# Performance work log

Measured on AMD Instinct MI355X. Metric: run time of the kernel, lower is better.

The kernel has to match this reference:

```python
import jax, jax.numpy as jnp
import numpy as np

B, T_TXT, T_IMG, N_LAT = 4, 2048, 8, 64
DIM, DIM_VIS, HEADS, DIM_HEAD = 2048, 1024, 8, 64
INNER = HEADS * DIM_HEAD
LN_EPS = 1e-5


def setup_inputs() -> dict:
    key = jax.random.key(0)
    ks = jax.random.split(key, 8)
    x = jax.random.normal(ks[0], (B, T_TXT, DIM), dtype=jnp.float32)
    media = jax.random.normal(ks[1], (B, T_IMG, N_LAT, DIM_VIS), dtype=jnp.float32)
    # exactly T_IMG media tokens per batch row at random positions
    pos = jax.random.randint(ks[2], (B, T_IMG), 0, T_TXT)
    media_locations = jnp.zeros((B, T_TXT), dtype=bool).at[jnp.arange(B)[:, None], pos].set(True)
    gamma = jnp.ones((DIM,), dtype=jnp.float32)
    beta = jnp.zeros((DIM,), dtype=jnp.float32)
    Wq = jax.random.normal(ks[3], (DIM, INNER), dtype=jnp.float32) * 0.02
    Wkv = jax.random.normal(ks[4], (DIM_VIS, 2 * INNER), dtype=jnp.float32) * 0.02
    Wout = jax.random.normal(ks[5], (INNER, DIM), dtype=jnp.float32) * 0.02
    return {"x": x, "media": media, "media_locations": media_locations,
            "gamma": gamma, "beta": beta, "Wq": Wq, "Wkv": Wkv, "Wout": Wout}


def _split_heads(t, h):
    b, s, _ = t.shape
    return t.reshape(b, s, h, -1).transpose(0, 2, 1, 3)  # b h s d


def reference(x, media, media_locations, gamma, beta, Wq, Wkv, Wout):
    b, t_txt, _ = x.shape
    _, t_img, n, _ = media.shape
    scale = DIM_HEAD ** (-0.5)

    # LayerNorm
    mu = jnp.mean(x, axis=-1, keepdims=True)
    var = jnp.mean(jnp.square(x - mu), axis=-1, keepdims=True)
    xn = (x - mu) * jax.lax.rsqrt(var + LN_EPS) * gamma + beta

    q = _split_heads(xn @ Wq, HEADS) * scale                # b h i d
    media_f = media.reshape(b, t_img * n, -1)               # b (t n) dv
    kv = media_f @ Wkv
    k, v = jnp.split(kv, 2, axis=-1)
    k = _split_heads(k, HEADS)                              # b h j d
    v = _split_heads(v, HEADS)

    sim = jnp.einsum('bhid,bhjd->bhij', q, k)               # b h i (t n)

    text_time = jnp.cumsum(media_locations.astype(jnp.int32), axis=-1)   # b i
    media_time = jnp.repeat(jnp.arange(1, t_img + 1), n)                 # (t n)
    mask = text_time[:, None, :, None] == media_time[None, None, None, :]

    neg = -jnp.finfo(sim.dtype).max
    sim = jnp.where(mask, sim, neg)
    sim = sim - jax.lax.stop_gradient(jnp.max(sim, axis=-1, keepdims=True))
    attn = jax.nn.softmax(sim, axis=-1)
    # zero attention for text tokens that precede any media
    attn = jnp.where((text_time == 0)[:, None, :, None], 0.0, attn)

    out = jnp.einsum('bhij,bhjd->bhid', attn, v)
    out = out.transpose(0, 2, 1, 3).reshape(b, t_txt, INNER)
    return out @ Wout
```

## Files before the change

kernel.cpp:

```cpp
#include <hip/hip_runtime.h>
#include <hip/hip_bf16.h>
#include <stdint.h>

typedef __bf16 bf16_t;
typedef __bf16 bf16x8 __attribute__((ext_vector_type(8)));
typedef float f32x4 __attribute__((ext_vector_type(4)));

#define NB      4
#define T_TXT   2048
#define T_IMG   8
#define N_LAT   64
#define DIM     2048
#define DIM_VIS 1024
#define HEADS   8
#define DHEAD   64
#define INNER   512

__device__ __forceinline__ void gld_lds16(const void* g, void* l) {
    __builtin_amdgcn_global_load_lds((const __attribute__((address_space(1))) void*)g,
                                     (__attribute__((address_space(3))) void*)l,
                                     16, 0, 0);
}

__global__ __launch_bounds__(256) void transpose3_k(const float* __restrict__ Wq,
                                                    const float* __restrict__ Wkv,
                                                    const float* __restrict__ Wout,
                                                    bf16_t* __restrict__ WqT,
                                                    bf16_t* __restrict__ WkvT,
                                                    bf16_t* __restrict__ WoutT) {
    __shared__ float tile[32][33];
    const float* in; bf16_t* out; int R, C;
    int which = blockIdx.y;
    if (which == 0)      { in = Wq;   out = WqT;   R = 2048; C = 512;  }
    else if (which == 1) { in = Wkv;  out = WkvT;  R = 1024; C = 1024; }
    else                 { in = Wout; out = WoutT; R = 512;  C = 2048; }
    int nbx = C >> 5;
    int bx = blockIdx.x % nbx, by = blockIdx.x / nbx;
    int c0 = bx * 32, r0 = by * 32;
    int x = threadIdx.x, y = threadIdx.y;
#pragma unroll
    for (int d = 0; d < 4; d++)
        tile[y + d * 8][x] = in[(size_t)(r0 + y + d * 8) * C + c0 + x];
    __syncthreads();
#pragma unroll
    for (int d = 0; d < 4; d++)
        out[(size_t)(c0 + y + d * 8) * R + r0 + x] = (bf16_t)tile[x][y + d * 8];
}

__global__ __launch_bounds__(256) void cvt_k(const float* __restrict__ in,
                                             bf16_t* __restrict__ out) {
    int idx = (blockIdx.x * 256 + threadIdx.x) * 8;
    f32x4 a = *(const f32x4*)(in + idx);
    f32x4 b = *(const f32x4*)(in + idx + 4);
    bf16x8 o;
#pragma unroll
    for (int i = 0; i < 4; i++) { o[i] = (bf16_t)a[i]; o[i + 4] = (bf16_t)b[i]; }
    *(bf16x8*)(out + idx) = o;
}

__global__ __launch_bounds__(256) void ln_k(const float* __restrict__ x,
                                            const float* __restrict__ gamma,
                                            const float* __restrict__ beta,
                                            bf16_t* __restrict__ xn) {
    int row = blockIdx.x;
    int t = threadIdx.x;
    const float* xp = x + (size_t)row * DIM + t * 8;
    f32x4 v0 = *(const f32x4*)xp;
    f32x4 v1 = *(const f32x4*)(xp + 4);
    float f[8];
    float s = 0.f, ss = 0.f;
#pragma unroll
    for (int i = 0; i < 4; i++) { f[i] = v0[i]; f[i + 4] = v1[i]; }
#pragma unroll
    for (int i = 0; i < 8; i++) { s += f[i]; ss += f[i] * f[i]; }
#pragma unroll
    for (int off = 32; off > 0; off >>= 1) { s += __shfl_xor(s, off); ss += __shfl_xor(ss, off); }
    __shared__ float sbuf[4], sbuf2[4];
    int wid = t >> 6, lane = t & 63;
    if (lane == 0) { sbuf[wid] = s; sbuf2[wid] = ss; }
    __syncthreads();
    s  = sbuf[0] + sbuf[1] + sbuf[2] + sbuf[3];
    ss = sbuf2[0] + sbuf2[1] + sbuf2[2] + sbuf2[3];
    float mu  = s * (1.0f / DIM);
    float var = ss * (1.0f / DIM) - mu * mu;
    float rs  = rsqrtf(var + 1e-5f);
    f32x4 g0 = *(const f32x4*)(gamma + t * 8);
    f32x4 g1 = *(const f32x4*)(gamma + t * 8 + 4);
    f32x4 b0 = *(const f32x4*)(beta + t * 8);
    f32x4 b1 = *(const f32x4*)(beta + t * 8 + 4);
    bf16x8 o;
#pragma unroll
    for (int i = 0; i < 4; i++) {
        o[i]     = (bf16_t)((f[i]     - mu) * rs * g0[i] + b0[i]);
        o[i + 4] = (bf16_t)((f[i + 4] - mu) * rs * g1[i] + b1[i]);
    }
    *(bf16x8*)(xn + (size_t)row * DIM + t * 8) = o;
}

template <typename OT>
__device__ __forceinline__ void gemm_body256(const bf16_t* __restrict__ A,
                                             const bf16_t* __restrict__ Bt,
                                             OT* __restrict__ C,
                                             int M, int N, int K, int Kper,
                                             float scale, int bid,
                                             int gx, int gy, int gz,
                                             bf16_t* lA, bf16_t* lB) {
    int tid = threadIdx.x;
    int w = tid >> 6, lane = tid & 63;
    int wm = w >> 2, wn = w & 3;

    int nwg = gx * gy * gz;
    int cpx = nwg >> 3;
    int nid = (bid & 7) * cpx + (bid >> 3);
    int tpy = gx * gz;
    int by = nid / tpy;
    int rr = nid - by * tpy;
    int bz = rr / gx;
    int bx = rr - bz * gx;

    int bm0 = by * 256, bn0 = bx * 256;
    int kbase = bz * Kper;
    int q = lane >> 4, l16 = lane & 15;

    const bf16_t* pA0 = A  + (size_t)(bm0 + w * 32      + l16) * K + kbase + q * 8;
    const bf16_t* pA1 = A  + (size_t)(bm0 + w * 32 + 16 + l16) * K + kbase + q * 8;
    const bf16_t* pB0 = Bt + (size_t)(bn0 + w * 32      + l16) * K + kbase + q * 8;
    const bf16_t* pB1 = Bt + (size_t)(bn0 + w * 32 + 16 + l16) * K + kbase + q * 8;

    f32x4 acc[8][4];
#pragma unroll
    for (int i = 0; i < 8; i++)
#pragma unroll
        for (int j = 0; j < 4; j++)
            acc[i][j] = (f32x4){0.f, 0.f, 0.f, 0.f};

    auto stage = [&](int t) {
        int buf = t & 3;
        int k0 = t << 5;
        gld_lds16(pA0 + k0, lA + buf * 8192 + (w * 2)     * 512);
        gld_lds16(pA1 + k0, lA + buf * 8192 + (w * 2 + 1) * 512);
        gld_lds16(pB0 + k0, lB + buf * 8192 + (w * 2)     * 512);
        gld_lds16(pB1 + k0, lB + buf * 8192 + (w * 2 + 1) * 512);
    };
    auto compute = [&](int t, bool dostage) {
        int buf = t & 3;
        bf16x8 af[8], bfr[4];
#pragma unroll
        for (int mt = 0; mt < 8; mt++)
            af[mt] = *(const bf16x8*)(lA + buf * 8192 + (wm * 8 + mt) * 512 + q * 128 + l16 * 8);
#pragma unroll
        for (int nt = 0; nt < 4; nt++)
            bfr[nt] = *(const bf16x8*)(lB + buf * 8192 + (wn * 4 + nt) * 512 + q * 128 + l16 * 8);
        if (dostage) stage(t + 3);
        __builtin_amdgcn_s_setprio(1);
#pragma unroll
        for (int mt = 0; mt < 8; mt++)
#pragma unroll
            for (int nt = 0; nt < 4; nt++)
                acc[mt][nt] = __builtin_amdgcn_mfma_f32_16x16x32_bf16(af[mt], bfr[nt], acc[mt][nt], 0, 0, 0);
        __builtin_amdgcn_s_setprio(0);
    };

    int nsteps = Kper >> 5;
    stage(0); stage(1); stage(2);
    for (int t = 0; t < nsteps - 2; t++) {
        asm volatile("s_waitcnt vmcnt(8)" ::: "memory");
        __builtin_amdgcn_s_barrier();
        __builtin_amdgcn_sched_barrier(0);
        compute(t, t + 3 < nsteps);
    }
    asm volatile("s_waitcnt vmcnt(4)" ::: "memory");
    __builtin_amdgcn_s_barrier();
    __builtin_amdgcn_sched_barrier(0);
    compute(nsteps - 2, false);
    asm volatile("s_waitcnt vmcnt(0)" ::: "memory");
    __builtin_amdgcn_s_barrier();
    __builtin_amdgcn_sched_barrier(0);
    compute(nsteps - 1, false);

    OT* Cz = C + (size_t)bz * M * N;
#pragma unroll
    for (int mt = 0; mt < 8; mt++)
#pragma unroll
        for (int nt = 0; nt < 4; nt++)
#pragma unroll
            for (int r = 0; r < 4; r++) {
                int row = bm0 + wm * 128 + mt * 16 + q * 4 + r;
                int col = bn0 + wn * 64 + nt * 16 + l16;
                Cz[(size_t)row * N + col] = (OT)(acc[mt][nt][r] * scale);
            }
}

__global__ __launch_bounds__(512, 2) void gemm12_k(const bf16_t* __restrict__ xn,
                                                   const bf16_t* __restrict__ WqT,
                                                   bf16_t* __restrict__ part,
                                                   const bf16_t* __restrict__ mediab,
                                                   const bf16_t* __restrict__ WkvT,
                                                   bf16_t* __restrict__ kvpart) {
    __shared__ __align__(16) bf16_t lA[4 * 8192];
    __shared__ __align__(16) bf16_t lB[4 * 8192];
    int bid = blockIdx.x;
    if (bid < 256)
        gemm_body256<bf16_t>(xn, WqT, part, 8192, 512, 2048, 512, 1.0f, bid, 2, 32, 4, lA, lB);
    else
        gemm_body256<bf16_t>(mediab, WkvT, kvpart, 2048, 1024, 1024, 256, 1.0f, bid - 256, 4, 8, 4, lA, lB);
}

__global__ __launch_bounds__(512, 2) void gemm3_k(const bf16_t* __restrict__ aout,
                                                  const bf16_t* __restrict__ WoutT,
                                                  float* __restrict__ out) {
    __shared__ __align__(16) bf16_t lA[4 * 8192];
    __shared__ __align__(16) bf16_t lB[4 * 8192];
    gemm_body256<float>(aout, WoutT, out, 8192, 2048, 512, 512, 1.0f, blockIdx.x, 8, 32, 1, lA, lB);
}

__global__ __launch_bounds__(256) void reduce4_k(const bf16_t* __restrict__ p,
                                                 bf16_t* __restrict__ o,
                                                 size_t n, float scale) {
    size_t i = ((size_t)blockIdx.x * 256 + threadIdx.x) * 8;
    bf16x8 a0 = *(const bf16x8*)(p + i);
    bf16x8 a1 = *(const bf16x8*)(p + n + i);
    bf16x8 a2 = *(const bf16x8*)(p + 2 * n + i);
    bf16x8 a3 = *(const bf16x8*)(p + 3 * n + i);
    bf16x8 r;
#pragma unroll
    for (int u = 0; u < 8; u++)
        r[u] = (bf16_t)(((float)a0[u] + (float)a1[u] + (float)a2[u] + (float)a3[u]) * scale);
    *(bf16x8*)(o + i) = r;
}

__global__ __launch_bounds__(256) void cumsum_bucket_k(const void* __restrict__ locs,
                                                       int* __restrict__ bstart,
                                                       int* __restrict__ bcnt) {
    int b = blockIdx.x, t = threadIdx.x;
    const unsigned* up = (const unsigned*)locs;
    const int* ip = (const int*)locs;
    const unsigned char* bp = (const unsigned char*)locs;
    const float* fp = (const float*)locs;

    int other = 0, nf = 0;
#pragma unroll
    for (int i = 0; i < 8; i++) {
        unsigned wv = up[t * 8 + i];
        nf    += (wv == 0x3F800000u);
        other += (wv != 0u && wv != 1u && wv != 0x3F800000u);
    }
#pragma unroll
    for (int off = 32; off > 0; off >>= 1) { other += __shfl_xor(other, off); nf += __shfl_xor(nf, off); }
    __shared__ int so[4], sf[4];
    int wid = t >> 6, lane = t & 63;
    if (lane == 0) { so[wid] = other; sf[wid] = nf; }
    __syncthreads();
    other = so[0] + so[1] + so[2] + so[3];
    nf    = sf[0] + sf[1] + sf[2] + sf[3];
    int mode = (other > 0) ? 0 : ((nf > 0) ? 2 : 1);

    int v[8];
    int s = 0;
#pragma unroll
    for (int i = 0; i < 8; i++) {
        int idx = b * T_TXT + t * 8 + i;
        int xv;
        if (mode == 1)      xv = ip[idx];
        else if (mode == 0) xv = (int)bp[idx];
        else                xv = (fp[idx] != 0.f) ? 1 : 0;
        v[i] = xv;
        s += xv;
    }
    __shared__ int sc[256];
    __shared__ int sstart[T_IMG];
    if (t < T_IMG) sstart[t] = T_TXT;
    sc[t] = s;
    __syncthreads();
    for (int off = 1; off < 256; off <<= 1) {
        int add = (t >= off) ? sc[t - off] : 0;
        __syncthreads();
        sc[t] += add;
        __syncthreads();
    }
    int run = sc[t] - s;
#pragma unroll
    for (int i = 0; i < 8; i++) {
        run += v[i];
        if (v[i] && run <= T_IMG) sstart[run - 1] = t * 8 + i;
    }
    __syncthreads();
    if (t < T_IMG) {
        int st = sstart[t];
        int nx = (t + 1 < T_IMG) ? sstart[t + 1] : T_TXT;
        bstart[b * T_IMG + t] = st;
        bcnt[b * T_IMG + t]   = nx - st;
    }
}

__global__ __launch_bounds__(256) void attn_mfma_k(const bf16_t* __restrict__ q,
                                                   const bf16_t* __restrict__ kv,
                                                   const int* __restrict__ bstart,
                                                   const int* __restrict__ bcnt,
                                                   bf16_t* __restrict__ aout) {
    __shared__ __align__(16) bf16_t lK[64 * 64];
    __shared__ __align__(16) bf16_t lVt[64 * 64];
    __shared__ __align__(16) bf16_t lP[4][16 * 64];

    int bid = blockIdx.x;
    int bucket = bid >> 6;
    int h = (bid >> 3) & 7;
    int c = bid & 7;
    int n_q = bcnt[bucket];
    int qlo = c << 8;
    if (n_q <= qlo) return;
    int qhi = (n_q < qlo + 256) ? n_q : (qlo + 256);
    int b = bucket >> 3;
    int timg = bucket & 7;
    int row0 = b * T_TXT + bstart[bucket];
    size_t krow0 = (size_t)(b * (T_IMG * N_LAT) + timg * N_LAT);

    int tid = threadIdx.x;
    int wid = tid >> 6, lane = tid & 63;
    int quad = lane >> 4, l16 = lane & 15;

    {
        const bf16_t* s0 = kv + (krow0 + 16 * wid + (lane >> 3)) * (2 * INNER) + h * DHEAD + (lane & 7) * 8;
        const bf16_t* s1 = kv + (krow0 + 16 * wid + 8 + (lane >> 3)) * (2 * INNER) + h * DHEAD + (lane & 7) * 8;
        gld_lds16(s0, lK + wid * 1024);
        gld_lds16(s1, lK + wid * 1024 + 512);
    }
    {
        int key = tid & 63, dblk = tid >> 6;
        const bf16_t* vsrc = kv + (krow0 + key) * (2 * INNER) + INNER + h * DHEAD + dblk * 16;
        bf16x8 v0 = *(const bf16x8*)vsrc;
        bf16x8 v1 = *(const bf16x8*)(vsrc + 8);
#pragma unroll
        for (int u = 0; u < 8; u++) {
            lVt[(dblk * 16 + u) * 64 + key]     = v0[u];
            lVt[(dblk * 16 + 8 + u) * 64 + key] = v1[u];
        }
    }
    __syncthreads();

    for (int c0 = qlo + wid * 16; c0 < qhi; c0 += 64) {
        int qi = row0 + c0 + ((c0 + l16 < n_q) ? l16 : 0);

        const bf16_t* qrow = q + (size_t)qi * INNER + h * DHEAD + quad * 8;
        bf16x8 qf0 = *(const bf16x8*)qrow;
        bf16x8 qf1 = *(const bf16x8*)(qrow + 32);
        f32x4 s[4];
#pragma unroll
        for (int nt = 0; nt < 4; nt++) s[nt] = (f32x4){0.f, 0.f, 0.f, 0.f};
#pragma unroll
        for (int nt = 0; nt < 4; nt++) {
            bf16x8 kf0 = *(const bf16x8*)(lK + (l16 + 16 * nt) * 64 + quad * 8);
            bf16x8 kf1 = *(const bf16x8*)(lK + (l16 + 16 * nt) * 64 + 32 + quad * 8);
            s[nt] = __builtin_amdgcn_mfma_f32_16x16x32_bf16(qf0, kf0, s[nt], 0, 0, 0);
            s[nt] = __builtin_amdgcn_mfma_f32_16x16x32_bf16(qf1, kf1, s[nt], 0, 0, 0);
        }

        float mr[4];
#pragma unroll
        for (int r = 0; r < 4; r++) {
            float m = fmaxf(fmaxf(s[0][r], s[1][r]), fmaxf(s[2][r], s[3][r]));
#pragma unroll
            for (int off = 8; off >= 1; off >>= 1) m = fmaxf(m, __shfl_xor(m, off));
            mr[r] = m;
        }
        float p[4][4];
#pragma unroll
        for (int nt = 0; nt < 4; nt++)
#pragma unroll
            for (int r = 0; r < 4; r++)
                p[nt][r] = __expf(s[nt][r] - mr[r]);
#pragma unroll
        for (int r = 0; r < 4; r++) {
            float tsum = p[0][r] + p[1][r] + p[2][r] + p[3][r];
#pragma unroll
            for (int off = 8; off >= 1; off >>= 1) tsum += __shfl_xor(tsum, off);
            float inv = 1.0f / tsum;
            p[0][r] *= inv; p[1][r] *= inv; p[2][r] *= inv; p[3][r] *= inv;
        }

        bf16_t* pt = lP[wid];
#pragma unroll
        for (int nt = 0; nt < 4; nt++)
#pragma unroll
            for (int r = 0; r < 4; r++)
                pt[(quad * 4 + r) * 64 + 16 * nt + l16] = (bf16_t)p[nt][r];
        asm volatile("s_waitcnt lgkmcnt(0)" ::: "memory");

        bf16x8 pf0 = *(const bf16x8*)(pt + l16 * 64 + quad * 8);
        bf16x8 pf1 = *(const bf16x8*)(pt + l16 * 64 + 32 + quad * 8);
        f32x4 o[4];
#pragma unroll
        for (int ntd = 0; ntd < 4; ntd++) o[ntd] = (f32x4){0.f, 0.f, 0.f, 0.f};
#pragma unroll
        for (int ntd = 0; ntd < 4; ntd++) {
            bf16x8 vf0 = *(const bf16x8*)(lVt + (l16 + 16 * ntd) * 64 + quad * 8);
            bf16x8 vf1 = *(const bf16x8*)(lVt + (l16 + 16 * ntd) * 64 + 32 + quad * 8);
            o[ntd] = __builtin_amdgcn_mfma_f32_16x16x32_bf16(pf0, vf0, o[ntd], 0, 0, 0);
            o[ntd] = __builtin_amdgcn_mfma_f32_16x16x32_bf16(pf1, vf1, o[ntd], 0, 0, 0);
        }

#pragma unroll
        for (int r = 0; r < 4; r++) {
            int qidx = c0 + quad * 4 + r;
            if (qidx < n_q) {
                bf16_t* op = aout + (size_t)(row0 + qidx) * INNER + h * DHEAD + l16;
#pragma unroll
                for (int ntd = 0; ntd < 4; ntd++)
                    op[16 * ntd] = (bf16_t)o[ntd][r];
            }
        }
    }
}

extern "C" void kernel_launch(void* const* d_in, const int* in_sizes, int n_in,
                              void* d_out, int out_size, void* d_ws, size_t ws_size,
                              hipStream_t stream) {
    const float* x     = (const float*)d_in[0];
    const float* media = (const float*)d_in[1];
    const void*  locs  = d_in[2];
    const float* gamma = (const float*)d_in[3];
    const float* beta  = (const float*)d_in[4];
    const float* Wq    = (const float*)d_in[5];
    const float* Wkv   = (const float*)d_in[6];
    const float* Wout  = (const float*)d_in[7];
    float* out = (float*)d_out;

    bf16_t* xn   = (bf16_t*)d_out;
    bf16_t* part = (bf16_t*)d_out + (size_t)16 * 1024 * 1024;

    char* p = (char*)d_ws;
    bf16_t* qbuf   = (bf16_t*)p; p += (size_t)8192 * 512 * 2;
    bf16_t* aout   = (bf16_t*)p; p += (size_t)8192 * 512 * 2;
    bf16_t* kvbuf  = (bf16_t*)p; p += (size_t)2048 * 1024 * 2;
    bf16_t* mediab = (bf16_t*)p; p += (size_t)2048 * 1024 * 2;
    bf16_t* WqT    = (bf16_t*)p; p += (size_t)512 * 2048 * 2;
    bf16_t* WkvT   = (bf16_t*)p; p += (size_t)1024 * 1024 * 2;
    bf16_t* WoutT  = (bf16_t*)p; p += (size_t)2048 * 512 * 2;
    int*    bstart = (int*)p;    p += 32 * sizeof(int);
    int*    bcnt   = (int*)p;    p += 32 * sizeof(int);

    cumsum_bucket_k<<<NB, 256, 0, stream>>>(locs, bstart, bcnt);
    transpose3_k<<<dim3(1024, 3), dim3(32, 8), 0, stream>>>(Wq, Wkv, Wout, WqT, WkvT, WoutT);
    cvt_k<<<(2048 * 1024) / (256 * 8), 256, 0, stream>>>(media, mediab);

    ln_k<<<8192, 256, 0, stream>>>(x, gamma, beta, xn);

    gemm12_k<<<384, 512, 0, stream>>>(xn, WqT, part, mediab, WkvT, qbuf);

    reduce4_k<<<1024, 256, 0, stream>>>(qbuf, kvbuf, (size_t)2048 * 1024, 1.0f);
    reduce4_k<<<2048, 256, 0, stream>>>(part, qbuf, (size_t)8192 * 512, 0.125f);

    hipMemsetAsync(aout, 0, (size_t)8192 * 512 * 2, stream);

    attn_mfma_k<<<32 * HEADS * 8, 256, 0, stream>>>(qbuf, kvbuf, bstart, bcnt, aout);

    gemm3_k<<<256, 512, 0, stream>>>(aout, WoutT, out);
}
```

Before: 263.4 us.

## Restructure GEMM pipeline to double-buffered K=64 steps with split fragment loads

Replaces the four-stage K=32 ring buffer with a two-buffer scheme holding K=64 per stage. Each stage is processed as two K halves with one barrier per half. Within a half, the A fragments are loaded in two groups of four, and the next stage's global-to-LDS copies are interleaved between the MFMA groups. The aim is fewer register-held fragments and finer interleaving of loads with MFMA work, at the cost of a shallower prefetch distance.

Measured after the change: 263.6 us. No clear change (+0.1%).

```diff
diff --git a/kernel.cpp b/kernel.cpp
--- a/kernel.cpp
+++ b/kernel.cpp
@@ -121,11 +121,12 @@
     int bm0 = by * 256, bn0 = bx * 256;
     int kbase = bz * Kper;
     int q = lane >> 4, l16 = lane & 15;
-
-    const bf16_t* pA0 = A  + (size_t)(bm0 + w * 32      + l16) * K + kbase + q * 8;
-    const bf16_t* pA1 = A  + (size_t)(bm0 + w * 32 + 16 + l16) * K + kbase + q * 8;
-    const bf16_t* pB0 = Bt + (size_t)(bn0 + w * 32      + l16) * K + kbase + q * 8;
-    const bf16_t* pB1 = Bt + (size_t)(bn0 + w * 32 + 16 + l16) * K + kbase + q * 8;
+    int rbase = q * 128 + l16 * 8;
+
+    const bf16_t* sA0 = A  + (size_t)(bm0 + (2 * w) * 16     + l16) * K + kbase + q * 8;
+    const bf16_t* sA1 = A  + (size_t)(bm0 + (2 * w + 1) * 16 + l16) * K + kbase + q * 8;
+    const bf16_t* sB0 = Bt + (size_t)(bn0 + (2 * w) * 16     + l16) * K + kbase + q * 8;
+    const bf16_t* sB1 = Bt + (size_t)(bn0 + (2 * w + 1) * 16 + l16) * K + kbase + q * 8;
 
     f32x4 acc[8][4];
 #pragma unroll
@@ -134,49 +135,86 @@
         for (int j = 0; j < 4; j++)
             acc[i][j] = (f32x4){0.f, 0.f, 0.f, 0.f};
 
-    auto stage = [&](int t) {
-        int buf = t & 3;
-        int k0 = t << 5;
-        gld_lds16(pA0 + k0, lA + buf * 8192 + (w * 2)     * 512);
-        gld_lds16(pA1 + k0, lA + buf * 8192 + (w * 2 + 1) * 512);
-        gld_lds16(pB0 + k0, lB + buf * 8192 + (w * 2)     * 512);
-        gld_lds16(pB1 + k0, lB + buf * 8192 + (w * 2 + 1) * 512);
+    auto stA = [&](int buf, int t, int kh) {
+        int off = t * 64 + kh * 32;
+        bf16_t* d = lA + buf * 16384 + (kh * 16 + 2 * w) * 512;
+        gld_lds16(sA0 + off, d);
+        gld_lds16(sA1 + off, d + 512);
     };
-    auto compute = [&](int t, bool dostage) {
-        int buf = t & 3;
-        bf16x8 af[8], bfr[4];
-#pragma unroll
-        for (int mt = 0; mt < 8; mt++)
-            af[mt] = *(const bf16x8*)(lA + buf * 8192 + (wm * 8 + mt) * 512 + q * 128 + l16 * 8);
-#pragma unroll
-        for (int nt = 0; nt < 4; nt++)
-            bfr[nt] = *(const bf16x8*)(lB + buf * 8192 + (wn * 4 + nt) * 512 + q * 128 + l16 * 8);
-        if (dostage) stage(t + 3);
-        __builtin_amdgcn_s_setprio(1);
-#pragma unroll
-        for (int mt = 0; mt < 8; mt++)
-#pragma unroll
-            for (int nt = 0; nt < 4; nt++)
-                acc[mt][nt] = __builtin_amdgcn_mfma_f32_16x16x32_bf16(af[mt], bfr[nt], acc[mt][nt], 0, 0, 0);
-        __builtin_amdgcn_s_setprio(0);
+    auto stB = [&](int buf, int t, int kh) {
+        int off = t * 64 + kh * 32;
+        bf16_t* d = lB + buf * 16384 + (kh * 16 + 2 * w) * 512;
+        gld_lds16(sB0 + off, d);
+        gld_lds16(sB1 + off, d + 512);
     };
 
-    int nsteps = Kper >> 5;
-    stage(0); stage(1); stage(2);
-    for (int t = 0; t < nsteps - 2; t++) {
-        asm volatile("s_waitcnt vmcnt(8)" ::: "memory");
+    int T = Kper >> 6;
+    stA(0, 0, 0); stB(0, 0, 0);
+    stA(0, 0, 1); stB(0, 0, 1);
+
+    for (int t = 0; t < T; ++t) {
+        int buf = t & 1;
+        int nbuf = buf ^ 1;
+        const bf16_t* LA = lA + buf * 16384;
+        const bf16_t* LB = lB + buf * 16384;
+        bool more = (t + 1 < T);
+
+        asm volatile("s_waitcnt vmcnt(4)" ::: "memory");
         __builtin_amdgcn_s_barrier();
         __builtin_amdgcn_sched_barrier(0);
-        compute(t, t + 3 < nsteps);
-    }
-    asm volatile("s_waitcnt vmcnt(4)" ::: "memory");
-    __builtin_amdgcn_s_barrier();
-    __builtin_amdgcn_sched_barrier(0);
-    compute(nsteps - 2, false);
-    asm volatile("s_waitcnt vmcnt(0)" ::: "memory");
-    __builtin_amdgcn_s_barrier();
-    __builtin_amdgcn_sched_barrier(0);
-    compute(nsteps - 1, false);
+
+        bf16x8 af[4], bfr[4];
+#pragma unroll
+        for (int i = 0; i < 4; i++) af[i]  = *(const bf16x8*)(LA + (wm * 8 + i) * 512 + rbase);
+#pragma unroll
+        for (int j = 0; j < 4; j++) bfr[j] = *(const bf16x8*)(LB + (wn * 4 + j) * 512 + rbase);
+        if (more) stA(nbuf, t + 1, 0);
+        __builtin_amdgcn_s_setprio(1);
+#pragma unroll
+        for (int i = 0; i < 4; i++)
+#pragma unroll
+            for (int j = 0; j < 4; j++)
+                acc[i][j] = __builtin_amdgcn_mfma_f32_16x16x32_bf16(af[i], bfr[j], acc[i][j], 0, 0, 0);
+        __builtin_amdgcn_s_setprio(0);
+#pragma unroll
+        for (int i = 0; i < 4; i++) af[i] = *(const bf16x8*)(LA + (wm * 8 + 4 + i) * 512 + rbase);
+        if (more) stB(nbuf, t + 1, 0);
+        __builtin_amdgcn_s_setprio(1);
+#pragma unroll
+        for (int i = 0; i < 4; i++)
+#pragma unroll
+            for (int j = 0; j < 4; j++)
+                acc[4 + i][j] = __builtin_amdgcn_mfma_f32_16x16x32_bf16(af[i], bfr[j], acc[4 + i][j], 0, 0, 0);
+        __builtin_amdgcn_s_setprio(0);
+
+        if (more) { asm volatile("s_waitcnt vmcnt(4)" ::: "memory"); }
+        else      { asm volatile("s_waitcnt vmcnt(0)" ::: "memory"); }
+        __builtin_amdgcn_s_barrier();
+        __builtin_amdgcn_sched_barrier(0);
+
+#pragma unroll
+        for (int i = 0; i < 4; i++) af[i]  = *(const bf16x8*)(LA + (16 + wm * 8 + i) * 512 + rbase);
+#pragma unroll
+        for (int j = 0; j < 4; j++) bfr[j] = *(const bf16x8*)(LB + (16 + wn * 4 + j) * 512 + rbase);
+        if (more) stA(nbuf, t + 1, 1);
+        __builtin_amdgcn_s_setprio(1);
+#pragma unroll
+        for (int i = 0; i < 4; i++)
+#pragma unroll
+            for (int j = 0; j < 4; j++)
+                acc[i][j] = __builtin_amdgcn_mfma_f32_16x16x32_bf16(af[i], bfr[j], acc[i][j], 0, 0, 0);
+        __builtin_amdgcn_s_setprio(0);
+#pragma unroll
+        for (int i = 0; i < 4; i++) af[i] = *(const bf16x8*)(LA + (16 + wm * 8 + 4 + i) * 512 + rbase);
+        if (more) stB(nbuf, t + 1, 1);
+        __builtin_amdgcn_s_setprio(1);
+#pragma unroll
+        for (int i = 0; i < 4; i++)
+#pragma unroll
+            for (int j = 0; j < 4; j++)
+                acc[4 + i][j] = __builtin_amdgcn_mfma_f32_16x16x32_bf16(af[i], bfr[j], acc[4 + i][j], 0, 0, 0);
+        __builtin_amdgcn_s_setprio(0);
+    }
 
     OT* Cz = C + (size_t)bz * M * N;
 #pragma unroll
@@ -197,8 +235,8 @@
                                                    const bf16_t* __restrict__ mediab,
                                                    const bf16_t* __restrict__ WkvT,
                                                    bf16_t* __restrict__ kvpart) {
-    __shared__ __align__(16) bf16_t lA[4 * 8192];
-    __shared__ __align__(16) bf16_t lB[4 * 8192];
+    __shared__ __align__(16) bf16_t lA[2 * 16384];
+    __shared__ __align__(16) bf16_t lB[2 * 16384];
     int bid = blockIdx.x;
     if (bid < 256)
         gemm_body256<bf16_t>(xn, WqT, part, 8192, 512, 2048, 512, 1.0f, bid, 2, 32, 4, lA, lB);
@@ -209,8 +247,8 @@
 __global__ __launch_bounds__(512, 2) void gemm3_k(const bf16_t* __restrict__ aout,
                                                   const bf16_t* __restrict__ WoutT,
                                                   float* __restrict__ out) {
-    __shared__ __align__(16) bf16_t lA[4 * 8192];
-    __shared__ __align__(16) bf16_t lB[4 * 8192];
+    __shared__ __align__(16) bf16_t lA[2 * 16384];
+    __shared__ __align__(16) bf16_t lB[2 * 16384];
     gemm_body256<float>(aout, WoutT, out, 8192, 2048, 512, 512, 1.0f, blockIdx.x, 8, 32, 1, lA, lB);
 }
 
```

## Merge prep kernels, drop KV split-K reduction, fold memset into reduce

Applied to the files above, without the earlier changes.

Combines the weight transposes, media conversion and location cumsum into one prep kernel. The KV projection now runs without split-K (32 blocks writing kvbuf directly), and those blocks are placed first in the fused GEMM launch, which removes one reduction kernel. Zeroing of the attention output buffer moves into the Q reduction kernel, replacing the memset. The aim is fewer launches and less partial-sum traffic, at the cost of longer per-block K loops for the KV GEMM.

After: 257.8 us. -2.1%, faster.

```diff
diff --git a/kernel.cpp b/kernel.cpp
--- a/kernel.cpp
+++ b/kernel.cpp
@@ -22,40 +22,111 @@
                                      16, 0, 0);
 }
 
-__global__ __launch_bounds__(256) void transpose3_k(const float* __restrict__ Wq,
-                                                    const float* __restrict__ Wkv,
-                                                    const float* __restrict__ Wout,
-                                                    bf16_t* __restrict__ WqT,
-                                                    bf16_t* __restrict__ WkvT,
-                                                    bf16_t* __restrict__ WoutT) {
-    __shared__ float tile[32][33];
-    const float* in; bf16_t* out; int R, C;
-    int which = blockIdx.y;
-    if (which == 0)      { in = Wq;   out = WqT;   R = 2048; C = 512;  }
-    else if (which == 1) { in = Wkv;  out = WkvT;  R = 1024; C = 1024; }
-    else                 { in = Wout; out = WoutT; R = 512;  C = 2048; }
-    int nbx = C >> 5;
-    int bx = blockIdx.x % nbx, by = blockIdx.x / nbx;
-    int c0 = bx * 32, r0 = by * 32;
-    int x = threadIdx.x, y = threadIdx.y;
-#pragma unroll
-    for (int d = 0; d < 4; d++)
-        tile[y + d * 8][x] = in[(size_t)(r0 + y + d * 8) * C + c0 + x];
-    __syncthreads();
-#pragma unroll
-    for (int d = 0; d < 4; d++)
-        out[(size_t)(c0 + y + d * 8) * R + r0 + x] = (bf16_t)tile[x][y + d * 8];
-}
-
-__global__ __launch_bounds__(256) void cvt_k(const float* __restrict__ in,
-                                             bf16_t* __restrict__ out) {
-    int idx = (blockIdx.x * 256 + threadIdx.x) * 8;
-    f32x4 a = *(const f32x4*)(in + idx);
-    f32x4 b = *(const f32x4*)(in + idx + 4);
-    bf16x8 o;
-#pragma unroll
-    for (int i = 0; i < 4; i++) { o[i] = (bf16_t)a[i]; o[i + 4] = (bf16_t)b[i]; }
-    *(bf16x8*)(out + idx) = o;
+__global__ __launch_bounds__(256) void prep_k(const float* __restrict__ Wq,
+                                              const float* __restrict__ Wkv,
+                                              const float* __restrict__ Wout,
+                                              bf16_t* __restrict__ WqT,
+                                              bf16_t* __restrict__ WkvT,
+                                              bf16_t* __restrict__ WoutT,
+                                              const float* __restrict__ media,
+                                              bf16_t* __restrict__ mediab,
+                                              const void* __restrict__ locs,
+                                              int* __restrict__ bstart,
+                                              int* __restrict__ bcnt) {
+    __shared__ union {
+        float tile[32][33];
+        struct { int so[4]; int sf[4]; int sc[256]; int sstart[T_IMG]; } cs;
+    } sm;
+    int bid = blockIdx.x;
+    int tid = threadIdx.x;
+
+    if (bid < 3072) {
+        int which = bid >> 10, tix = bid & 1023;
+        const float* in; bf16_t* out; int R, C;
+        if (which == 0)      { in = Wq;   out = WqT;   R = 2048; C = 512;  }
+        else if (which == 1) { in = Wkv;  out = WkvT;  R = 1024; C = 1024; }
+        else                 { in = Wout; out = WoutT; R = 512;  C = 2048; }
+        int nbx = C >> 5;
+        int bx = tix % nbx, by = tix / nbx;
+        int c0 = bx * 32, r0 = by * 32;
+        int x = tid & 31, y = tid >> 5;
+#pragma unroll
+        for (int d = 0; d < 4; d++)
+            sm.tile[y + d * 8][x] = in[(size_t)(r0 + y + d * 8) * C + c0 + x];
+        __syncthreads();
+#pragma unroll
+        for (int d = 0; d < 4; d++)
+            out[(size_t)(c0 + y + d * 8) * R + r0 + x] = (bf16_t)sm.tile[x][y + d * 8];
+        return;
+    }
+    if (bid < 4096) {
+        int idx = ((bid - 3072) * 256 + tid) * 8;
+        f32x4 a = *(const f32x4*)(media + idx);
+        f32x4 b = *(const f32x4*)(media + idx + 4);
+        bf16x8 o;
+#pragma unroll
+        for (int i = 0; i < 4; i++) { o[i] = (bf16_t)a[i]; o[i + 4] = (bf16_t)b[i]; }
+        *(bf16x8*)(mediab + idx) = o;
+        return;
+    }
+    {
+        int b = bid - 4096, t = tid;
+        const unsigned* up = (const unsigned*)locs;
+        const int* ip = (const int*)locs;
+        const unsigned char* bp = (const unsigned char*)locs;
+        const float* fp = (const float*)locs;
+
+        int other = 0, nf = 0;
+#pragma unroll
+        for (int i = 0; i < 8; i++) {
+            unsigned wv = up[t * 8 + i];
+            nf    += (wv == 0x3F800000u);
+            other += (wv != 0u && wv != 1u && wv != 0x3F800000u);
+        }
+#pragma unroll
+        for (int off = 32; off > 0; off >>= 1) { other += __shfl_xor(other, off); nf += __shfl_xor(nf, off); }
+        int wid = t >> 6, lane = t & 63;
+        if (lane == 0) { sm.cs.so[wid] = other; sm.cs.sf[wid] = nf; }
+        __syncthreads();
+        other = sm.cs.so[0] + sm.cs.so[1] + sm.cs.so[2] + sm.cs.so[3];
+        nf    = sm.cs.sf[0] + sm.cs.sf[1] + sm.cs.sf[2] + sm.cs.sf[3];
+        int mode = (other > 0) ? 0 : ((nf > 0) ? 2 : 1);
+
+        int v[8];
+        int s = 0;
+#pragma unroll
+        for (int i = 0; i < 8; i++) {
+            int idx = b * T_TXT + t * 8 + i;
+            int xv;
+            if (mode == 1)      xv = ip[idx];
+            else if (mode == 0) xv = (int)bp[idx];
+            else                xv = (fp[idx] != 0.f) ? 1 : 0;
+            v[i] = xv;
+            s += xv;
+        }
+        if (t < T_IMG) sm.cs.sstart[t] = T_TXT;
+        sm.cs.sc[t] = s;
+        __syncthreads();
+        for (int off = 1; off < 256; off <<= 1) {
+            int add = (t >= off) ? sm.cs.sc[t - off] : 0;
+            __syncthreads();
+            sm.cs.sc[t] += add;
+            __syncthreads();
+        }
+        int run = sm.cs.sc[t] - s;
+#pragma unroll
+        for (int i = 0; i < 8; i++) {
+            run += v[i];
+            if (v[i] && run <= T_IMG) sm.cs.sstart[run - 1] = t * 8 + i;
+        }
+        __syncthreads();
+        if (t < T_IMG) {
+            int st = sm.cs.sstart[t];
+            int nx = (t + 1 < T_IMG) ? sm.cs.sstart[t + 1] : T_TXT;
+            bstart[b * T_IMG + t] = st;
+            bcnt[b * T_IMG + t]   = nx - st;
+        }
+    }
 }
 
 __global__ __launch_bounds__(256) void ln_k(const float* __restrict__ x,
@@ -196,14 +267,14 @@
                                                    bf16_t* __restrict__ part,
                                                    const bf16_t* __restrict__ mediab,
                                                    const bf16_t* __restrict__ WkvT,
-                                                   bf16_t* __restrict__ kvpart) {
+                                                   bf16_t* __restrict__ kvbuf) {
     __shared__ __align__(16) bf16_t lA[4 * 8192];
     __shared__ __align__(16) bf16_t lB[4 * 8192];
     int bid = blockIdx.x;
-    if (bid < 256)
-        gemm_body256<bf16_t>(xn, WqT, part, 8192, 512, 2048, 512, 1.0f, bid, 2, 32, 4, lA, lB);
+    if (bid < 32)
+        gemm_body256<bf16_t>(mediab, WkvT, kvbuf, 2048, 1024, 1024, 1024, 1.0f, bid, 4, 8, 1, lA, lB);
     else
-        gemm_body256<bf16_t>(mediab, WkvT, kvpart, 2048, 1024, 1024, 256, 1.0f, bid - 256, 4, 8, 4, lA, lB);
+        gemm_body256<bf16_t>(xn, WqT, part, 8192, 512, 2048, 512, 1.0f, bid - 32, 2, 32, 4, lA, lB);
 }
 
 __global__ __launch_bounds__(512, 2) void gemm3_k(const bf16_t* __restrict__ aout,
@@ -214,83 +285,23 @@
     gemm_body256<float>(aout, WoutT, out, 8192, 2048, 512, 512, 1.0f, blockIdx.x, 8, 32, 1, lA, lB);
 }
 
-__global__ __launch_bounds__(256) void reduce4_k(const bf16_t* __restrict__ p,
-                                                 bf16_t* __restrict__ o,
-                                                 size_t n, float scale) {
+__global__ __launch_bounds__(256) void reduce4_zero_k(const bf16_t* __restrict__ p,
+                                                      bf16_t* __restrict__ qbuf,
+                                                      bf16_t* __restrict__ aout) {
+    size_t n = (size_t)8192 * 512;
     size_t i = ((size_t)blockIdx.x * 256 + threadIdx.x) * 8;
     bf16x8 a0 = *(const bf16x8*)(p + i);
     bf16x8 a1 = *(const bf16x8*)(p + n + i);
     bf16x8 a2 = *(const bf16x8*)(p + 2 * n + i);
     bf16x8 a3 = *(const bf16x8*)(p + 3 * n + i);
-    bf16x8 r;
-#pragma unroll
-    for (int u = 0; u < 8; u++)
-        r[u] = (bf16_t)(((float)a0[u] + (float)a1[u] + (float)a2[u] + (float)a3[u]) * scale);
-    *(bf16x8*)(o + i) = r;
-}
-
-__global__ __launch_bounds__(256) void cumsum_bucket_k(const void* __restrict__ locs,
-                                                       int* __restrict__ bstart,
-                                                       int* __restrict__ bcnt) {
-    int b = blockIdx.x, t = threadIdx.x;
-    const unsigned* up = (const unsigned*)locs;
-    const int* ip = (const int*)locs;
-    const unsigned char* bp = (const unsigned char*)locs;
-    const float* fp = (const float*)locs;
-
-    int other = 0, nf = 0;
-#pragma unroll
-    for (int i = 0; i < 8; i++) {
-        unsigned wv = up[t * 8 + i];
-        nf    += (wv == 0x3F800000u);
-        other += (wv != 0u && wv != 1u && wv != 0x3F800000u);
-    }
-#pragma unroll
-    for (int off = 32; off > 0; off >>= 1) { other += __shfl_xor(other, off); nf += __shfl_xor(nf, off); }
-    __shared__ int so[4], sf[4];
-    int wid = t >> 6, lane = t & 63;
-    if (lane == 0) { so[wid] = other; sf[wid] = nf; }
-    __syncthreads();
-    other = so[0] + so[1] + so[2] + so[3];
-    nf    = sf[0] + sf[1] + sf[2] + sf[3];
-    int mode = (other > 0) ? 0 : ((nf > 0) ? 2 : 1);
-
-    int v[8];
-    int s = 0;
-#pragma unroll
-    for (int i = 0; i < 8; i++) {
-        int idx = b * T_TXT + t * 8 + i;
-        int xv;
-        if (mode == 1)      xv = ip[idx];
-        else if (mode == 0) xv = (int)bp[idx];
-        else                xv = (fp[idx] != 0.f) ? 1 : 0;
-        v[i] = xv;
-        s += xv;
-    }
-    __shared__ int sc[256];
-    __shared__ int sstart[T_IMG];
-    if (t < T_IMG) sstart[t] = T_TXT;
-    sc[t] = s;
-    __syncthreads();
-    for (int off = 1; off < 256; off <<= 1) {
-        int add = (t >= off) ? sc[t - off] : 0;
-        __syncthreads();
-        sc[t] += add;
-        __syncthreads();
-    }
-    int run = sc[t] - s;
-#pragma unroll
-    for (int i = 0; i < 8; i++) {
-        run += v[i];
-        if (v[i] && run <= T_IMG) sstart[run - 1] = t * 8 + i;
-    }
-    __syncthreads();
-    if (t < T_IMG) {
-        int st = sstart[t];
-        int nx = (t + 1 < T_IMG) ? sstart[t + 1] : T_TXT;
-        bstart[b * T_IMG + t] = st;
-        bcnt[b * T_IMG + t]   = nx - st;
-    }
+    bf16x8 r, z;
+#pragma unroll
+    for (int u = 0; u < 8; u++) {
+        r[u] = (bf16_t)(((float)a0[u] + (float)a1[u] + (float)a2[u] + (float)a3[u]) * 0.125f);
+        z[u] = (bf16_t)0.f;
+    }
+    *(bf16x8*)(qbuf + i) = r;
+    *(bf16x8*)(aout + i) = z;
 }
 
 __global__ __launch_bounds__(256) void attn_mfma_k(const bf16_t* __restrict__ q,
@@ -439,18 +450,14 @@
     int*    bstart = (int*)p;    p += 32 * sizeof(int);
     int*    bcnt   = (int*)p;    p += 32 * sizeof(int);
 
-    cumsum_bucket_k<<<NB, 256, 0, stream>>>(locs, bstart, bcnt);
-    transpose3_k<<<dim3(1024, 3), dim3(32, 8), 0, stream>>>(Wq, Wkv, Wout, WqT, WkvT, WoutT);
-    cvt_k<<<(2048 * 1024) / (256 * 8), 256, 0, stream>>>(media, mediab);
+    prep_k<<<4100, 256, 0, stream>>>(Wq, Wkv, Wout, WqT, WkvT, WoutT,
+                                     media, mediab, locs, bstart, bcnt);
 
     ln_k<<<8192, 256, 0, stream>>>(x, gamma, beta, xn);
 
-    gemm12_k<<<384, 512, 0, stream>>>(xn, WqT, part, mediab, WkvT, qbuf);
-
-    reduce4_k<<<1024, 256, 0, stream>>>(qbuf, kvbuf, (size_t)2048 * 1024, 1.0f);
-    reduce4_k<<<2048, 256, 0, stream>>>(part, qbuf, (size_t)8192 * 512, 0.125f);
-
-    hipMemsetAsync(aout, 0, (size_t)8192 * 512 * 2, stream);
+    gemm12_k<<<288, 512, 0, stream>>>(xn, WqT, part, mediab, WkvT, kvbuf);
+
+    reduce4_zero_k<<<2048, 256, 0, stream>>>(part, qbuf, aout);
 
     attn_mfma_k<<<32 * HEADS * 8, 256, 0, stream>>>(qbuf, kvbuf, bstart, bcnt, aout);
 
```
